# Kernel optimization log

Hardware: AMD Instinct MI355X
Metric: run time of the kernel (lower is better)

The kernel has to match this reference:

```python
import jax, jax.numpy as jnp
from jax import lax
import numpy as np

NS, NQ = 115, 23          # support / query node counts (1 node per graph here)
GS, GQ, C = 115, 23, 23   # support graphs (5-shot x 23-way), query graphs, classes
D = 1024


def _seg_mean(x, idx, n):
    # scatter-mean along axis 0 (matches torch_scatter reduce='mean'; empty segments -> 0)
    s = jax.ops.segment_sum(x, idx, num_segments=n)
    cnt = jax.ops.segment_sum(jnp.ones(x.shape[0], x.dtype), idx, num_segments=n)
    return s / jnp.maximum(cnt, 1.0).reshape((n,) + (1,) * (x.ndim - 1))


def _cnn(x, cw1, cb1, cw_rest, cb_rest):
    def block(h, w, b):
        h = lax.conv_general_dilated(h, w, (1, 1), 'SAME',
                                     dimension_numbers=('NCHW', 'OIHW', 'NCHW'))
        h = jax.nn.relu(h + b[None, :, None, None])
        return lax.reduce_window(h, -jnp.inf, lax.max, (1, 1, 2, 2), (1, 1, 2, 2), 'VALID')
    x = block(x, cw1, cb1)
    for i in range(cw_rest.shape[0]):
        x = block(x, cw_rest[i], cb_rest[i])
    return x.reshape(x.shape[0], -1)  # [N, 1024]


def _agg_mean(x, edge_index, n):
    # PyG propagate: message x_j = x[src], scatter-mean onto dst
    return _seg_mean(x[edge_index[0]], edge_index[1], n)


def setup_inputs() -> dict:
    key = jax.random.key(0)
    ks = jax.random.split(key, 12)
    s = 0.05
    return {
        'support_x': jax.random.normal(ks[0], (NS, 3, 256, 256), jnp.float32),
        'support_edge_index': jax.random.randint(ks[1], (2, 4096), 0, NS),
        'support_batch': jnp.arange(NS),          # 1 node per support graph
        'support_y': jnp.arange(GS) // 5,         # 5 graphs per class, classes 0..22
        'query_x': jax.random.normal(ks[2], (NQ, 3, 256, 256), jnp.float32),
        'query_edge_index': jax.random.randint(ks[3], (2, 1024), 0, NQ),
        'query_batch': jnp.arange(NQ),            # 1 node per query graph
        'query_y': jax.random.randint(ks[4], (GQ,), 0, C),
        'center': jax.random.normal(ks[5], (C, D), jnp.float32),
        'cw1': jax.random.normal(ks[6], (64, 3, 3, 3), jnp.float32) * s,
        'cb1': jnp.zeros((64,), jnp.float32),
        'cw_rest': jax.random.normal(ks[7], (5, 64, 64, 3, 3), jnp.float32) * s,
        'cb_rest': jnp.zeros((5, 64), jnp.float32),
        'lin2_w': jax.random.normal(ks[8], (D, D), jnp.float32) * 0.03,   # [in,out]
        'lin2_b': jnp.zeros((D,), jnp.float32),
        'mlp_w': jax.random.normal(ks[9], (2 * D, D), jnp.float32) * 0.02,  # [in,out]
        'mlp_b': jnp.zeros((D,), jnp.float32),
    }


def reference(support_x, support_edge_index, support_batch, support_y,
              query_x, query_edge_index, query_batch, query_y, center,
              cw1, cb1, cw_rest, cb_rest, lin2_w, lin2_b, mlp_w, mlp_b):
    n_cls = center.shape[0]

    def feats(x, ei):
        n = x.shape[0]
        h1 = _cnn(x, cw1, cb1, cw_rest, cb_rest)          # conv1 s_x1 = x (flatten feats)
        sx = _agg_mean(h1, ei, n) * h1                    # conv1 update: agg * x
        h2 = sx @ lin2_w + lin2_b                         # conv2 Linear(1024,1024)
        h2 = _agg_mean(h2, ei, n) * h2                    # conv2 update: agg * x
        return jnp.concatenate([h1, h2], axis=-1) @ mlp_w + mlp_b  # [N, 1024]

    s_x = feats(support_x, support_edge_index)            # [Ns, D]
    q_x = feats(query_x, query_edge_index)                # [Nq, D]
    gs = support_y.shape[0]
    gq = query_y.shape[0]

    # per-query-node RBF distances, scatter-mean over support graphs, log-softmax over D
    a = jnp.exp(-(s_x[None, :, :] - q_x[:, None, :]) ** 2)        # [Nq, Ns, D]
    a = _seg_mean(jnp.transpose(a, (1, 0, 2)), support_batch, gs) # [Gs, Nq, D]
    pd = jax.nn.log_softmax(jnp.transpose(a, (1, 0, 2)), axis=-1) # [Nq, Gs, D]

    s_xg = _seg_mean(s_x, support_batch, gs)              # [Gs, D]
    q_xg = _seg_mean(q_x, query_batch, gq)                # [Gq, D]
    pd = _seg_mean(pd, query_batch, gq)                   # [Gq, Gs, D]

    s_c = 0.25 * jnp.repeat(center, 5, axis=0) + 0.5 * s_xg       # [Gs, D]
    b = (jnp.exp(-(s_c[None, :, :] - q_xg[:, None, :]) ** 2) + pd).sum(-1)  # [Gq, Gs]
    b = jax.nn.log_softmax(b, axis=-1)
    dis = _seg_mean(b.T, support_y, n_cls).T              # [Gq, C]

    center_new = _seg_mean(s_xg, support_y, n_cls) * 0.5 + 0.25 * center

    y = jax.nn.one_hot(query_y, n_cls, dtype=jnp.float32)
    loss = -(y * jax.nn.log_softmax(dis, axis=-1)).sum()  # F.cross_entropy(soft, sum)
    acc = (jnp.argmax(dis, axis=1) == query_y).astype(jnp.float32).sum()
    return loss, acc, center_new
```

## Files before the change

kernel.cpp:

```cpp
#include <hip/hip_runtime.h>
#include <cstdint>
#include <cstddef>


typedef _Float16 f16x8 __attribute__((ext_vector_type(8)));
typedef __attribute__((ext_vector_type(4))) float f32x4;

#define WL 36864

__global__ __launch_bounds__(256)
void wtransform(const float* __restrict__ cwr, const float* __restrict__ cw1,
                _Float16* __restrict__ wbuf5, _Float16* __restrict__ w1buf) {
  int i = blockIdx.x * 256 + threadIdx.x;
  if (i < 184320) {
    int layer = i / 36864; int rem = i - layer * 36864;
    int tap = rem / 4096;  int r2 = rem - tap * 4096;
    int cc = r2 / 2048;    int r3 = r2 - cc * 2048;
    int nt = r3 / 512;     int r4 = r3 - nt * 512;
    int lane = r4 / 8;     int j = r4 - lane * 8;
    int ic = cc * 32 + (lane >> 4) * 8 + j;
    int oc = nt * 16 + (lane & 15);
    float w = cwr[(((size_t)layer * 64 + oc) * 64 + ic) * 9 + tap];
    wbuf5[(size_t)layer * 36864 + tap * 4096 + (cc * 4 + nt) * 512 + lane * 8 + j] =
        (_Float16)w;
  } else if (i < 184320 + 2048) {
    int e = i - 184320;
    int nt = e / 512; int r4 = e - nt * 512;
    int lane = r4 / 8; int j = r4 - lane * 8;
    int k = (lane >> 4) * 8 + j;
    float w = 0.f;
    if (k < 27) {
      int tap = k / 3, ic = k - tap * 3;
      int oc = nt * 16 + (lane & 15);
      w = cw1[((size_t)oc * 3 + ic) * 9 + tap];
    }
    w1buf[nt * 512 + lane * 8 + j] = (_Float16)w;
  }
}

__global__ __launch_bounds__(256)
void wtransform_lin(const float* __restrict__ w, _Float16* __restrict__ frag,
                    int KS) {
  int i = blockIdx.x * 256 + threadIdx.x;
  int total = KS * 64 * 512;
  if (i >= total) return;
  int ks = i / (64 * 512); int rem = i - ks * (64 * 512);
  int nt = rem / 512;      int r = rem - nt * 512;
  int lane = r / 8;        int j = r - lane * 8;
  int k = ks * 32 + (lane >> 4) * 8 + j;
  int n = nt * 16 + (lane & 15);
  frag[((size_t)ks * 64 + nt) * 512 + lane * 8 + j] = (_Float16)w[(size_t)k * 1024 + n];
}

template<int KTOT>
__global__ __launch_bounds__(256)
void gemm_mfma(const float* __restrict__ A1, const float* __restrict__ A2,
               const _Float16* __restrict__ frag,
               const float* __restrict__ bias, float* __restrict__ out, int M) {
  __shared__ f32x4 s_red[4][4][64];
  const int tid = threadIdx.x;
  const int wave = tid >> 6, lane = tid & 63;
  const int q = lane >> 4, ml = lane & 15;
  const int m0 = blockIdx.y * 16;
  const int nb = blockIdx.x;
  int row = m0 + ml; if (row >= M) row = M - 1;

  f32x4 acc[4];
#pragma unroll
  for (int nt = 0; nt < 4; ++nt) acc[nt] = (f32x4){0.f, 0.f, 0.f, 0.f};

  constexpr int KSW = KTOT / 128;
  const int ksBase = wave * KSW;
#pragma unroll 2
  for (int s = 0; s < KSW; ++s) {
    int ks = ksBase + s;
    int k0 = ks * 32 + q * 8;
    const float* ap;
    if constexpr (KTOT == 2048) {
      ap = (k0 >= 1024) ? (A2 + (size_t)row * 1024 + (k0 - 1024))
                        : (A1 + (size_t)row * 1024 + k0);
    } else {
      ap = A1 + (size_t)row * 1024 + k0;
    }
    float4 va = *(const float4*)ap;
    float4 vb = *(const float4*)(ap + 4);
    f16x8 av;
    av[0] = (_Float16)va.x; av[1] = (_Float16)va.y;
    av[2] = (_Float16)va.z; av[3] = (_Float16)va.w;
    av[4] = (_Float16)vb.x; av[5] = (_Float16)vb.y;
    av[6] = (_Float16)vb.z; av[7] = (_Float16)vb.w;
    const _Float16* fb = frag + ((size_t)ks * 64 + nb * 4) * 512 + lane * 8;
#pragma unroll
    for (int nt = 0; nt < 4; ++nt) {
      f16x8 bv = *(const f16x8*)(fb + nt * 512);
      acc[nt] = __builtin_amdgcn_mfma_f32_16x16x32_f16(av, bv, acc[nt], 0, 0, 0);
    }
  }
#pragma unroll
  for (int nt = 0; nt < 4; ++nt) s_red[wave][nt][lane] = acc[nt];
  __syncthreads();
  {
    int nt = wave;
    f32x4 sum = s_red[0][nt][lane];
#pragma unroll
    for (int w2 = 1; w2 < 4; ++w2) {
      f32x4 p = s_red[w2][nt][lane];
      sum[0] += p[0]; sum[1] += p[1]; sum[2] += p[2]; sum[3] += p[3];
    }
    int n = nb * 64 + nt * 16 + ml;
    float bv = bias[n];
#pragma unroll
    for (int r = 0; r < 4; ++r) {
      int m = m0 + q * 4 + r;
      if (m < M) out[(size_t)m * 1024 + n] = sum[r] + bv;
    }
  }
}

template<int TCX, int TCY, bool FP32OUT>
__global__ __launch_bounds__(256, 3)
void conv_mfma(const _Float16* __restrict__ act_in,
               void* __restrict__ act_out,
               const _Float16* __restrict__ wbuf,
               const float* __restrict__ bias,
               int IH, int IW) {
  constexpr int PX = TCX + 2, PY = TCY + 2;
  constexpr int MT = (TCX * TCY) / 64;
  __shared__ __align__(16) _Float16 s_patch[PY * PX * 72];

  const int tid = threadIdx.x;
  const int wave = tid >> 6, lane = tid & 63;
  const int q = lane >> 4, ml = lane & 15;
  const int x0 = blockIdx.x * TCX, y0 = blockIdx.y * TCY;
  const int img = blockIdx.z;

  for (int u = tid; u < PY * PX * 8; u += 256) {
    int pos = u >> 3, sub = u & 7;
    int py = pos / PX, px = pos - py * PX;
    int gy = y0 - 1 + py, gx = x0 - 1 + px;
    uint4 v = {0u, 0u, 0u, 0u};
    if ((unsigned)gy < (unsigned)IH && (unsigned)gx < (unsigned)IW)
      v = *(const uint4*)(act_in + (((size_t)img * IH + gy) * IW + gx) * 64 + sub * 8);
    *(uint4*)(s_patch + pos * 72 + sub * 8) = v;
  }
  __syncthreads();

  f32x4 acc[MT][4];
#pragma unroll
  for (int mt = 0; mt < MT; ++mt)
#pragma unroll
    for (int nt = 0; nt < 4; ++nt)
      acc[mt][nt] = (f32x4){0.f, 0.f, 0.f, 0.f};

  int pxv[MT], pyv[MT];
#pragma unroll
  for (int mt = 0; mt < MT; ++mt) {
    int p = (wave * MT + mt) * 16 + ml;
    pxv[mt] = p % TCX;
    pyv[mt] = p / TCX;
  }

#pragma unroll 1
  for (int tap = 0; tap < 9; ++tap) {
    const _Float16* wt = wbuf + tap * 4096 + lane * 8;
    const int dy = tap / 3, dx = tap - dy * 3;
#pragma unroll
    for (int cc = 0; cc < 2; ++cc) {
      f16x8 bv[4];
#pragma unroll
      for (int nt = 0; nt < 4; ++nt)
        bv[nt] = *(const f16x8*)(wt + (cc * 4 + nt) * 512);
#pragma unroll
      for (int mt = 0; mt < MT; ++mt) {
        const _Float16* ap =
            s_patch + ((pyv[mt] + dy) * PX + (pxv[mt] + dx)) * 72 + cc * 32 + q * 8;
        f16x8 av = *(const f16x8*)ap;
#pragma unroll
        for (int nt = 0; nt < 4; ++nt)
          acc[mt][nt] = __builtin_amdgcn_mfma_f32_16x16x32_f16(av, bv[nt], acc[mt][nt], 0, 0, 0);
      }
    }
  }

  const int OH = IH >> 1, OW = IW >> 1;
#pragma unroll
  for (int nt = 0; nt < 4; ++nt) {
    int oc = nt * 16 + ml;
    float bvs = bias[oc];
    if constexpr (TCX == 16) {
#pragma unroll
      for (int mh = 0; mh < MT / 2; ++mh)
#pragma unroll
        for (int rh = 0; rh < 2; ++rh) {
          float a0 = fmaxf(acc[2 * mh][nt][2 * rh] + bvs, 0.f);
          float a1 = fmaxf(acc[2 * mh][nt][2 * rh + 1] + bvs, 0.f);
          float a2 = fmaxf(acc[2 * mh + 1][nt][2 * rh] + bvs, 0.f);
          float a3 = fmaxf(acc[2 * mh + 1][nt][2 * rh + 1] + bvs, 0.f);
          float m = fmaxf(fmaxf(a0, a1), fmaxf(a2, a3));
          int gy = (y0 >> 1) + wave * (MT / 2) + mh;
          int gx = (x0 >> 1) + q * 2 + rh;
          if (FP32OUT)
            ((float*)act_out)[(((size_t)img * 64 + oc) * OH + gy) * OW + gx] = m;
          else
            ((_Float16*)act_out)[(((size_t)img * OH + gy) * OW + gx) * 64 + oc] =
                (_Float16)m;
        }
    } else {
      float m01 = fmaxf(fmaxf(acc[0][nt][0] + bvs, 0.f), fmaxf(acc[0][nt][1] + bvs, 0.f));
      float m23 = fmaxf(fmaxf(acc[0][nt][2] + bvs, 0.f), fmaxf(acc[0][nt][3] + bvs, 0.f));
      float p0 = fmaxf(m01, __shfl_xor(m01, 32));
      float p1 = fmaxf(m23, __shfl_xor(m23, 32));
      if ((lane & 32) == 0) {
        int gy = (y0 >> 1) + wave;
        int gx0 = (x0 >> 1) + (q & 1) * 2;
        if (FP32OUT) {
          float* o = (float*)act_out + (((size_t)img * 64 + oc) * OH + gy) * OW + gx0;
          o[0] = p0; o[1] = p1;
        } else {
          _Float16* o = (_Float16*)act_out;
          o[(((size_t)img * OH + gy) * OW + gx0) * 64 + oc] = (_Float16)p0;
          o[(((size_t)img * OH + gy) * OW + gx0 + 1) * 64 + oc] = (_Float16)p1;
        }
      }
    }
  }
}

__global__ __launch_bounds__(256, 4)
void conv_l1(const float* __restrict__ in, _Float16* __restrict__ act_out,
             const _Float16* __restrict__ w1buf, const float* __restrict__ bias) {
  __shared__ __align__(16) char smem[20288];
  float* s_raw = (float*)smem;
  _Float16* s_im = (_Float16*)(smem + 3904);

  const int tid = threadIdx.x;
  const int wave = tid >> 6, lane = tid & 63;
  const int q = lane >> 4, ml = lane & 15;
  const int x0 = blockIdx.x * 16, y0 = blockIdx.y * 16;
  const int img = blockIdx.z;

  for (int i = tid; i < 972; i += 256) {
    int ic = i / 324, rem = i - ic * 324;
    int yy = rem / 18, xx = rem - yy * 18;
    int gy = y0 - 1 + yy, gx = x0 - 1 + xx;
    float v = 0.f;
    if ((unsigned)gy < 256u && (unsigned)gx < 256u)
      v = in[((size_t)img * 3 + ic) * 65536 + gy * 256 + gx];
    s_raw[i] = v;
  }
  __syncthreads();
  for (int e = tid; e < 8192; e += 256) {
    int t = e >> 9, r5 = e & 511;
    int lidx = r5 >> 3, j = r5 & 7;
    int m = lidx & 15, qq = lidx >> 4;
    int k = qq * 8 + j;
    float v = 0.f;
    if (k < 27) {
      int tap = k / 3, ic = k - tap * 3;
      int ddy = tap / 3, ddx = tap - ddy * 3;
      v = s_raw[ic * 324 + (t + ddy) * 18 + (m + ddx)];
    }
    s_im[e] = (_Float16)v;
  }
  __syncthreads();

  f16x8 bv[4];
#pragma unroll
  for (int nt = 0; nt < 4; ++nt)
    bv[nt] = *(const f16x8*)(w1buf + nt * 512 + lane * 8);

  f32x4 acc[4][4];
#pragma unroll
  for (int t4 = 0; t4 < 4; ++t4)
#pragma unroll
    for (int nt = 0; nt < 4; ++nt)
      acc[t4][nt] = (f32x4){0.f, 0.f, 0.f, 0.f};

#pragma unroll
  for (int t4 = 0; t4 < 4; ++t4) {
    int t = wave * 4 + t4;
    f16x8 av = *(const f16x8*)(s_im + t * 512 + lane * 8);
#pragma unroll
    for (int nt = 0; nt < 4; ++nt)
      acc[t4][nt] = __builtin_amdgcn_mfma_f32_16x16x32_f16(av, bv[nt], acc[t4][nt], 0, 0, 0);
  }

#pragma unroll
  for (int nt = 0; nt < 4; ++nt) {
    int oc = nt * 16 + ml;
    float bvs = bias[oc];
#pragma unroll
    for (int mh = 0; mh < 2; ++mh)
#pragma unroll
      for (int rh = 0; rh < 2; ++rh) {
        float a0 = fmaxf(acc[2 * mh][nt][2 * rh] + bvs, 0.f);
        float a1 = fmaxf(acc[2 * mh][nt][2 * rh + 1] + bvs, 0.f);
        float a2 = fmaxf(acc[2 * mh + 1][nt][2 * rh] + bvs, 0.f);
        float a3 = fmaxf(acc[2 * mh + 1][nt][2 * rh + 1] + bvs, 0.f);
        float m = fmaxf(fmaxf(a0, a1), fmaxf(a2, a3));
        int gy = blockIdx.y * 8 + wave * 2 + mh;
        int gx = blockIdx.x * 8 + q * 2 + rh;
        act_out[(((size_t)img * 128 + gy) * 128 + gx) * 64 + oc] = (_Float16)m;
      }
  }
}

__global__ __launch_bounds__(256)
void edge_agg_mul(const float* __restrict__ h, const int* __restrict__ ei,
                  int E, float* __restrict__ out) {
  __shared__ int list[1024];
  __shared__ int cnt;
  const int n = blockIdx.x;
  const int tid = threadIdx.x;
  if (tid == 0) cnt = 0;
  __syncthreads();
  for (int e = tid; e < E; e += 256) {
    if (ei[E + e] == n) {
      int p = atomicAdd(&cnt, 1);
      list[p] = ei[e];
    }
  }
  __syncthreads();
  const int c = cnt;
  float ax = 0.f, ay = 0.f, az = 0.f, aw = 0.f;
#pragma unroll 4
  for (int i = 0; i < c; ++i) {
    const float4 v = ((const float4*)(h + (size_t)list[i] * 1024))[tid];
    ax += v.x; ay += v.y; az += v.z; aw += v.w;
  }
  float inv = 1.f / (float)(c > 0 ? c : 1);
  const float4 hv = ((const float4*)(h + (size_t)n * 1024))[tid];
  float4 o;
  o.x = ax * inv * hv.x; o.y = ay * inv * hv.y;
  o.z = az * inv * hv.z; o.w = aw * inv * hv.w;
  ((float4*)(out + (size_t)n * 1024))[tid] = o;
}

__global__ __launch_bounds__(256)
void rbf_pairs(const float* __restrict__ sx, const float* __restrict__ qx,
               const float* __restrict__ center, float* __restrict__ bpre) {
  int gid = blockIdx.x * 256 + threadIdx.x;
  int wid = gid >> 6;
  int lane = gid & 63;
  if (wid >= 23 * 115) return;
  int qq = wid / 115, s = wid - qq * 115;
  const float* sr = sx + (size_t)s * 1024;
  const float* qr = qx + (size_t)qq * 1024;
  const float* cr = center + (size_t)(s / 5) * 1024;
  float S1 = 0.f, S2 = 0.f, S3 = 0.f;
  for (int d = lane; d < 1024; d += 64) {
    float sv = sr[d], qv = qr[d];
    float df = sv - qv;
    float a = expf(-df * df);
    S1 += a;
    S2 += expf(a);
    float sc = 0.25f * cr[d] + 0.5f * sv;
    float d2 = sc - qv;
    S3 += expf(-d2 * d2);
  }
#pragma unroll
  for (int o = 32; o > 0; o >>= 1) {
    S1 += __shfl_down(S1, o);
    S2 += __shfl_down(S2, o);
    S3 += __shfl_down(S3, o);
  }
  if (lane == 0) bpre[wid] = S3 + S1 - 1024.f * logf(S2);
}

__global__ __launch_bounds__(256)
void center_new_k(const float* __restrict__ sx, const float* __restrict__ center,
                  const int* __restrict__ sy, float* __restrict__ out) {
  __shared__ int syv[115];
  int tid = threadIdx.x;
  if (tid < 115) syv[tid] = sy[tid];
  __syncthreads();
  int c = blockIdx.x;
  int d = blockIdx.y * 256 + tid;
  float sum = 0.f; int cnt = 0;
  for (int s = 0; s < 115; ++s)
    if (syv[s] == c) { sum += sx[(size_t)s * 1024 + d]; ++cnt; }
  out[2 + (size_t)c * 1024 + d] =
      0.5f * (sum / (float)(cnt > 0 ? cnt : 1)) + 0.25f * center[(size_t)c * 1024 + d];
}

__global__ __launch_bounds__(256)
void finalize_k(const float* __restrict__ bpre, const int* __restrict__ sy,
                const int* __restrict__ qy, float* __restrict__ out) {
  __shared__ float bls[23][115];
  __shared__ float dis[23][23];
  __shared__ int   syv[115];
  __shared__ float ccnt[23];
  __shared__ float lossq[23];
  __shared__ float accq[23];
  const int tid = threadIdx.x;
  if (tid < 115) syv[tid] = sy[tid];
  __syncthreads();
  if (tid < 23) {
    float mx = -3.4e38f;
    for (int s = 0; s < 115; ++s) mx = fmaxf(mx, bpre[tid * 115 + s]);
    float se = 0.f;
    for (int s = 0; s < 115; ++s) se += expf(bpre[tid * 115 + s] - mx);
    float lse = mx + logf(se);
    for (int s = 0; s < 115; ++s) bls[tid][s] = bpre[tid * 115 + s] - lse;
    int c = 0;
    for (int s = 0; s < 115; ++s) c += (syv[s] == tid);
    ccnt[tid] = (float)(c > 0 ? c : 1);
  }
  __syncthreads();
  for (int i = tid; i < 23 * 23; i += 256) {
    int qq = i / 23, c = i - qq * 23;
    float sum = 0.f;
    for (int s = 0; s < 115; ++s)
      if (syv[s] == c) sum += bls[qq][s];
    dis[qq][c] = sum / ccnt[c];
  }
  __syncthreads();
  if (tid < 23) {
    int qq = tid;
    float mx = -3.4e38f; int am = 0;
    for (int c = 0; c < 23; ++c) {
      float v = dis[qq][c];
      if (v > mx) { mx = v; am = c; }
    }
    float se = 0.f;
    for (int c = 0; c < 23; ++c) se += expf(dis[qq][c] - mx);
    float lse = mx + logf(se);
    int y = qy[qq];
    lossq[qq] = -(dis[qq][y] - lse);
    accq[qq] = (am == y) ? 1.f : 0.f;
  }
  __syncthreads();
  if (tid == 0) {
    float L = 0.f, A = 0.f;
    for (int qq = 0; qq < 23; ++qq) { L += lossq[qq]; A += accq[qq]; }
    out[0] = L;
    out[1] = A;
  }
}

extern "C" void kernel_launch(void* const* d_in, const int* in_sizes, int n_in,
                              void* d_out, int out_size, void* d_ws, size_t ws_size,
                              hipStream_t stream) {
  const float* sup_x  = (const float*)d_in[0];
  const int*   sup_ei = (const int*)d_in[1];
  const int*   sup_y  = (const int*)d_in[3];
  const float* q_x    = (const float*)d_in[4];
  const int*   q_ei   = (const int*)d_in[5];
  const int*   q_y    = (const int*)d_in[7];
  const float* center = (const float*)d_in[8];
  const float* cw1    = (const float*)d_in[9];
  const float* cb1    = (const float*)d_in[10];
  const float* cwr    = (const float*)d_in[11];
  const float* cbr    = (const float*)d_in[12];
  const float* l2w    = (const float*)d_in[13];
  const float* l2b    = (const float*)d_in[14];
  const float* mw     = (const float*)d_in[15];
  const float* mb     = (const float*)d_in[16];
  float* out = (float*)d_out;

  char* base = (char*)d_ws;
  size_t off = 0;
  auto alloc = [&](size_t n) { char* p = base + off; off += (n + 255) & ~(size_t)255; return p; };
  _Float16* wbuf5 = (_Float16*)alloc(5 * WL * 2);
  _Float16* w1buf = (_Float16*)alloc(2048 * 2);
  float* h1   = (float*)alloc(138 * 1024 * 4);
  float* sxb  = (float*)alloc(138 * 1024 * 4);
  float* h2p  = (float*)alloc(138 * 1024 * 4);
  float* h2   = (float*)alloc(138 * 1024 * 4);
  float* feat = (float*)alloc(138 * 1024 * 4);
  float* bpre = (float*)alloc(23 * 115 * 4);

  const size_t BIG_R1 = 138ull * 64 * 64 * 64 * 2;
  const size_t BIG_R0 = 23ull * 128 * 128 * 64 * 2;
  const size_t SML_R1 = 12ull * 64 * 64 * 64 * 2;
  const size_t SML_R0 = 12ull * 128 * 128 * 64 * 2;
  const bool big = ws_size >= off + BIG_R1 + BIG_R0 + 4096;
  _Float16* region1 = (_Float16*)alloc(big ? BIG_R1 : SML_R1);
  _Float16* region0 = (_Float16*)alloc(big ? BIG_R0 : SML_R0);
  _Float16* l3out = region0;
  _Float16* l4out = region0 + (big ? 9043968u : 786432u);
  _Float16* l5out = region0 + (big ? 11304960u : 983040u);
  _Float16* wlin2 = region0;
  _Float16* wmlp  = region0 + 1048576u;

  wtransform<<<728, 256, 0, stream>>>(cwr, cw1, wbuf5, w1buf);

  if (big) {
    for (int c = 0; c < 6; ++c) {
      const float* xin = (c < 5) ? (sup_x + (size_t)c * 23 * 3 * 65536) : q_x;
      conv_l1<<<dim3(16, 16, 23), 256, 0, stream>>>(xin, region0, w1buf, cb1);
      conv_mfma<16, 16, false><<<dim3(8, 8, 23), 256, 0, stream>>>(
          region0, region1 + (size_t)c * 23 * 64 * 64 * 64, wbuf5, cbr, 128, 128);
    }
    conv_mfma<16, 16, false><<<dim3(4, 4, 138), 256, 0, stream>>>(
        region1, l3out, wbuf5 + 1 * WL, cbr + 64, 64, 64);
    conv_mfma<16, 16, false><<<dim3(2, 2, 138), 256, 0, stream>>>(
        l3out, l4out, wbuf5 + 2 * WL, cbr + 128, 32, 32);
    conv_mfma<16, 16, false><<<dim3(1, 1, 138), 256, 0, stream>>>(
        l4out, l5out, wbuf5 + 3 * WL, cbr + 192, 16, 16);
    conv_mfma<8, 8, true><<<dim3(1, 1, 138), 256, 0, stream>>>(
        l5out, h1, wbuf5 + 4 * WL, cbr + 256, 8, 8);
  } else {
    auto run_chain = [&](const float* xin, int n, int gb) {
      conv_l1<<<dim3(16, 16, n), 256, 0, stream>>>(xin, region0, w1buf, cb1);
      conv_mfma<16, 16, false><<<dim3(8, 8, n), 256, 0, stream>>>(
          region0, region1, wbuf5, cbr, 128, 128);
      conv_mfma<16, 16, false><<<dim3(4, 4, n), 256, 0, stream>>>(
          region1, l3out, wbuf5 + 1 * WL, cbr + 64, 64, 64);
      conv_mfma<16, 16, false><<<dim3(2, 2, n), 256, 0, stream>>>(
          l3out, l4out, wbuf5 + 2 * WL, cbr + 128, 32, 32);
      conv_mfma<16, 16, false><<<dim3(1, 1, n), 256, 0, stream>>>(
          l4out, l5out, wbuf5 + 3 * WL, cbr + 192, 16, 16);
      conv_mfma<8, 8, true><<<dim3(1, 1, n), 256, 0, stream>>>(
          l5out, h1 + (size_t)gb * 1024, wbuf5 + 4 * WL, cbr + 256, 8, 8);
    };
    for (int i0 = 0; i0 < 115; i0 += 12)
      run_chain(sup_x + (size_t)i0 * 3 * 65536, (115 - i0 < 12) ? 115 - i0 : 12, i0);
    for (int i0 = 0; i0 < 23; i0 += 12)
      run_chain(q_x + (size_t)i0 * 3 * 65536, (23 - i0 < 12) ? 23 - i0 : 12, 115 + i0);
  }

  wtransform_lin<<<4096, 256, 0, stream>>>(l2w, wlin2, 32);
  wtransform_lin<<<8192, 256, 0, stream>>>(mw, wmlp, 64);

  edge_agg_mul<<<115, 256, 0, stream>>>(h1, sup_ei, 4096, sxb);
  edge_agg_mul<<<23, 256, 0, stream>>>(h1 + 115 * 1024, q_ei, 1024, sxb + 115 * 1024);
  gemm_mfma<1024><<<dim3(16, 9), 256, 0, stream>>>(sxb, nullptr, wlin2, l2b, h2p, 138);
  edge_agg_mul<<<115, 256, 0, stream>>>(h2p, sup_ei, 4096, h2);
  edge_agg_mul<<<23, 256, 0, stream>>>(h2p + 115 * 1024, q_ei, 1024, h2 + 115 * 1024);
  gemm_mfma<2048><<<dim3(16, 9), 256, 0, stream>>>(h1, h2, wmlp, mb, feat, 138);

  rbf_pairs<<<(23 * 115 * 64 + 255) / 256, 256, 0, stream>>>(
      feat, feat + 115 * 1024, center, bpre);
  center_new_k<<<dim3(23, 4), 256, 0, stream>>>(feat, center, sup_y, out);
  finalize_k<<<1, 256, 0, stream>>>(bpre, sup_y, q_y, out);
}
```

Baseline: 812.4 us.

## Prefetch conv weights per tap, widen GEMM grid, batch first conv layers

The conv kernel now preloads all 8 weight fragments for the next tap into registers while MFMAs run on the current tap, so weight loads are double-buffered instead of issued inside the inner loop. The linear GEMMs now give each block 32 output columns instead of 64, doubling the grid for more parallelism. A new workspace tier runs the first two conv layers over all 115 support images in one launch when memory allows, cutting launch count. Prefetching raises register pressure under the 3-blocks launch bound, and the full tier needs a much larger workspace.

New measurement: 793.8 us. 1.02x faster.

```diff
diff --git a/kernel.cpp b/kernel.cpp
--- a/kernel.cpp
+++ b/kernel.cpp
@@ -57,7 +57,7 @@
 void gemm_mfma(const float* __restrict__ A1, const float* __restrict__ A2,
                const _Float16* __restrict__ frag,
                const float* __restrict__ bias, float* __restrict__ out, int M) {
-  __shared__ f32x4 s_red[4][4][64];
+  __shared__ f32x4 s_red[4][2][64];
   const int tid = threadIdx.x;
   const int wave = tid >> 6, lane = tid & 63;
   const int q = lane >> 4, ml = lane & 15;
@@ -65,9 +65,9 @@
   const int nb = blockIdx.x;
   int row = m0 + ml; if (row >= M) row = M - 1;
 
-  f32x4 acc[4];
-#pragma unroll
-  for (int nt = 0; nt < 4; ++nt) acc[nt] = (f32x4){0.f, 0.f, 0.f, 0.f};
+  f32x4 acc[2];
+#pragma unroll
+  for (int nt = 0; nt < 2; ++nt) acc[nt] = (f32x4){0.f, 0.f, 0.f, 0.f};
 
   constexpr int KSW = KTOT / 128;
   const int ksBase = wave * KSW;
@@ -89,17 +89,17 @@
     av[2] = (_Float16)va.z; av[3] = (_Float16)va.w;
     av[4] = (_Float16)vb.x; av[5] = (_Float16)vb.y;
     av[6] = (_Float16)vb.z; av[7] = (_Float16)vb.w;
-    const _Float16* fb = frag + ((size_t)ks * 64 + nb * 4) * 512 + lane * 8;
-#pragma unroll
-    for (int nt = 0; nt < 4; ++nt) {
+    const _Float16* fb = frag + ((size_t)ks * 64 + nb * 2) * 512 + lane * 8;
+#pragma unroll
+    for (int nt = 0; nt < 2; ++nt) {
       f16x8 bv = *(const f16x8*)(fb + nt * 512);
       acc[nt] = __builtin_amdgcn_mfma_f32_16x16x32_f16(av, bv, acc[nt], 0, 0, 0);
     }
   }
 #pragma unroll
-  for (int nt = 0; nt < 4; ++nt) s_red[wave][nt][lane] = acc[nt];
-  __syncthreads();
-  {
+  for (int nt = 0; nt < 2; ++nt) s_red[wave][nt][lane] = acc[nt];
+  __syncthreads();
+  if (wave < 2) {
     int nt = wave;
     f32x4 sum = s_red[0][nt][lane];
 #pragma unroll
@@ -107,7 +107,7 @@
       f32x4 p = s_red[w2][nt][lane];
       sum[0] += p[0]; sum[1] += p[1]; sum[2] += p[2]; sum[3] += p[3];
     }
-    int n = nb * 64 + nt * 16 + ml;
+    int n = nb * 32 + nt * 16 + ml;
     float bv = bias[n];
 #pragma unroll
     for (int r = 0; r < 4; ++r) {
@@ -143,6 +143,12 @@
       v = *(const uint4*)(act_in + (((size_t)img * IH + gy) * IW + gx) * 64 + sub * 8);
     *(uint4*)(s_patch + pos * 72 + sub * 8) = v;
   }
+
+  const _Float16* wl = wbuf + lane * 8;
+  f16x8 bw[8], bn[8];
+#pragma unroll
+  for (int f = 0; f < 8; ++f) bw[f] = *(const f16x8*)(wl + f * 512);
+
   __syncthreads();
 
   f32x4 acc[MT][4];
@@ -162,14 +168,14 @@
 
 #pragma unroll 1
   for (int tap = 0; tap < 9; ++tap) {
-    const _Float16* wt = wbuf + tap * 4096 + lane * 8;
+    if (tap < 8) {
+      const _Float16* np = wl + (tap + 1) * 4096;
+#pragma unroll
+      for (int f = 0; f < 8; ++f) bn[f] = *(const f16x8*)(np + f * 512);
+    }
     const int dy = tap / 3, dx = tap - dy * 3;
 #pragma unroll
     for (int cc = 0; cc < 2; ++cc) {
-      f16x8 bv[4];
-#pragma unroll
-      for (int nt = 0; nt < 4; ++nt)
-        bv[nt] = *(const f16x8*)(wt + (cc * 4 + nt) * 512);
 #pragma unroll
       for (int mt = 0; mt < MT; ++mt) {
         const _Float16* ap =
@@ -177,9 +183,12 @@
         f16x8 av = *(const f16x8*)ap;
 #pragma unroll
         for (int nt = 0; nt < 4; ++nt)
-          acc[mt][nt] = __builtin_amdgcn_mfma_f32_16x16x32_f16(av, bv[nt], acc[mt][nt], 0, 0, 0);
+          acc[mt][nt] = __builtin_amdgcn_mfma_f32_16x16x32_f16(av, bw[cc * 4 + nt],
+                                                               acc[mt][nt], 0, 0, 0);
       }
     }
+#pragma unroll
+    for (int f = 0; f < 8; ++f) bw[f] = bn[f];
   }
 
   const int OH = IH >> 1, OW = IW >> 1;
@@ -470,22 +479,41 @@
   float* feat = (float*)alloc(138 * 1024 * 4);
   float* bpre = (float*)alloc(23 * 115 * 4);
 
-  const size_t BIG_R1 = 138ull * 64 * 64 * 64 * 2;
-  const size_t BIG_R0 = 23ull * 128 * 128 * 64 * 2;
-  const size_t SML_R1 = 12ull * 64 * 64 * 64 * 2;
-  const size_t SML_R0 = 12ull * 128 * 128 * 64 * 2;
-  const bool big = ws_size >= off + BIG_R1 + BIG_R0 + 4096;
-  _Float16* region1 = (_Float16*)alloc(big ? BIG_R1 : SML_R1);
-  _Float16* region0 = (_Float16*)alloc(big ? BIG_R0 : SML_R0);
+  const size_t R1_FULL = 138ull * 64 * 64 * 64 * 2;
+  const size_t R0_FULL = 115ull * 128 * 128 * 64 * 2;
+  const size_t R0_23   = 23ull * 128 * 128 * 64 * 2;
+  const size_t R1_SML  = 12ull * 64 * 64 * 64 * 2;
+  const size_t R0_SML  = 12ull * 128 * 128 * 64 * 2;
+
+  const int tier = (ws_size >= off + R1_FULL + R0_FULL + 4096) ? 0
+                 : (ws_size >= off + R1_FULL + R0_23 + 4096)   ? 1 : 2;
+
+  _Float16* region1 = (_Float16*)alloc(tier <= 1 ? R1_FULL : R1_SML);
+  _Float16* region0 = (_Float16*)alloc(tier == 0 ? R0_FULL : (tier == 1 ? R0_23 : R0_SML));
   _Float16* l3out = region0;
-  _Float16* l4out = region0 + (big ? 9043968u : 786432u);
-  _Float16* l5out = region0 + (big ? 11304960u : 983040u);
+  _Float16* l4out = region0 + (tier <= 1 ? 9043968u : 786432u);
+  _Float16* l5out = region0 + (tier <= 1 ? 11304960u : 983040u);
   _Float16* wlin2 = region0;
   _Float16* wmlp  = region0 + 1048576u;
 
   wtransform<<<728, 256, 0, stream>>>(cwr, cw1, wbuf5, w1buf);
 
-  if (big) {
+  if (tier == 0) {
+    conv_l1<<<dim3(16, 16, 115), 256, 0, stream>>>(sup_x, region0, w1buf, cb1);
+    conv_mfma<16, 16, false><<<dim3(8, 8, 115), 256, 0, stream>>>(
+        region0, region1, wbuf5, cbr, 128, 128);
+    conv_l1<<<dim3(16, 16, 23), 256, 0, stream>>>(q_x, region0, w1buf, cb1);
+    conv_mfma<16, 16, false><<<dim3(8, 8, 23), 256, 0, stream>>>(
+        region0, region1 + 115ull * 64 * 64 * 64, wbuf5, cbr, 128, 128);
+    conv_mfma<16, 16, false><<<dim3(4, 4, 138), 256, 0, stream>>>(
+        region1, l3out, wbuf5 + 1 * WL, cbr + 64, 64, 64);
+    conv_mfma<16, 16, false><<<dim3(2, 2, 138), 256, 0, stream>>>(
+        l3out, l4out, wbuf5 + 2 * WL, cbr + 128, 32, 32);
+    conv_mfma<16, 16, false><<<dim3(1, 1, 138), 256, 0, stream>>>(
+        l4out, l5out, wbuf5 + 3 * WL, cbr + 192, 16, 16);
+    conv_mfma<8, 8, true><<<dim3(1, 1, 138), 256, 0, stream>>>(
+        l5out, h1, wbuf5 + 4 * WL, cbr + 256, 8, 8);
+  } else if (tier == 1) {
     for (int c = 0; c < 6; ++c) {
       const float* xin = (c < 5) ? (sup_x + (size_t)c * 23 * 3 * 65536) : q_x;
       conv_l1<<<dim3(16, 16, 23), 256, 0, stream>>>(xin, region0, w1buf, cb1);
@@ -525,10 +553,10 @@
 
   edge_agg_mul<<<115, 256, 0, stream>>>(h1, sup_ei, 4096, sxb);
   edge_agg_mul<<<23, 256, 0, stream>>>(h1 + 115 * 1024, q_ei, 1024, sxb + 115 * 1024);
-  gemm_mfma<1024><<<dim3(16, 9), 256, 0, stream>>>(sxb, nullptr, wlin2, l2b, h2p, 138);
+  gemm_mfma<1024><<<dim3(32, 9), 256, 0, stream>>>(sxb, nullptr, wlin2, l2b, h2p, 138);
   edge_agg_mul<<<115, 256, 0, stream>>>(h2p, sup_ei, 4096, h2);
   edge_agg_mul<<<23, 256, 0, stream>>>(h2p + 115 * 1024, q_ei, 1024, h2 + 115 * 1024);
-  gemm_mfma<2048><<<dim3(16, 9), 256, 0, stream>>>(h1, h2, wmlp, mb, feat, 138);
+  gemm_mfma<2048><<<dim3(32, 9), 256, 0, stream>>>(h1, h2, wmlp, mb, feat, 138);
 
   rbf_pairs<<<(23 * 115 * 64 + 255) / 256, 256, 0, stream>>>(
       feat, feat + 115 * 1024, center, bpre);
```
